# Kernel optimization log

Measured on AMD Instinct MI355X. Metric: run time of the kernel, lower is better.

Reference implementation:

```python
import jax, jax.numpy as jnp
import numpy as np

NUM_VIEW = 300
NSAMPLE = 1024
EPS = 1e-5


def generate_grasp_views(n):
    # golden-spiral views on the unit sphere (graspnetAPI.generate_grasp_views)
    phi = (np.sqrt(5.0) - 1.0) / 2.0
    i = np.arange(n)
    zi = (2 * i + 1) / n - 1
    ri = np.sqrt(np.maximum(1 - zi ** 2, 0))
    xi = ri * np.cos(2 * np.pi * i * phi)
    yi = ri * np.sin(2 * np.pi * i * phi)
    return jnp.asarray(np.stack([xi, yi, zi], axis=-1).astype(np.float32))


def viewpoint_to_matrix(towards):
    # batch_viewpoint_params_to_matrix with angle=0 -> R1 = I
    axis_x = towards  # [M,3]
    axis_y = jnp.stack([-axis_x[:, 1], axis_x[:, 0], jnp.zeros_like(axis_x[:, 0])], axis=-1)
    ny = jnp.linalg.norm(axis_y, axis=-1, keepdims=True)
    axis_y = jnp.where(ny == 0, jnp.array([0.0, 1.0, 0.0], dtype=towards.dtype), axis_y)
    axis_x = axis_x / jnp.linalg.norm(axis_x, axis=-1, keepdims=True)
    axis_y = axis_y / jnp.linalg.norm(axis_y, axis=-1, keepdims=True)
    axis_z = jnp.cross(axis_x, axis_y)
    return jnp.stack([axis_x, axis_y, axis_z], axis=-1)  # columns = axes


def conv1x1(x, w, b):
    # x [B,C,N], w [O,C], b [O] -> [B,O,N]
    return jnp.einsum('oc,bcn->bon', w, x) + b[None, :, None]


def bn(x, g, be, m, v):
    # inference-mode BatchNorm1d over channel dim
    return (x - m[None, :, None]) * (g / jnp.sqrt(v + EPS))[None, :, None] + be[None, :, None]


def masked_fps(xyz, mask):
    # furthest point sampling restricted to mask==True; equivalent to running
    # standard FPS on the compacted point set (same points, same distances,
    # same selection order, indices expressed in original coordinates).
    big = jnp.float32(1e10)
    dist0 = jnp.where(mask, big, jnp.float32(-1.0))
    start = jnp.argmax(mask)  # first valid index == compacted index 0

    def step(carry, _):
        dist, cur = carry
        d = jnp.sum((xyz - xyz[cur]) ** 2, axis=-1)
        dist = jnp.where(mask, jnp.minimum(dist, d), jnp.float32(-1.0))
        nxt = jnp.argmax(dist)
        return (dist, nxt), cur

    _, inds = jax.lax.scan(step, (dist0, start), None, length=NSAMPLE)
    return inds  # [NSAMPLE]


def setup_inputs() -> dict:
    key = jax.random.key(0)
    ks = jax.random.split(key, 32)
    B, N, C, V = 4, 20000, 256, 300
    s = 0.05
    rn = lambda k, sh, sc=1.0: jax.random.normal(k, sh, jnp.float32) * sc
    rv = lambda k, sh: jax.random.uniform(k, sh, jnp.float32) + 0.5
    return {
        'seed_xyz': jax.random.uniform(ks[0], (B, N, 3), jnp.float32),
        'seed_features': rn(ks[1], (B, C, N)),
        # graspable_head: conv-bn-relu-conv
        'gh_w1': rn(ks[2], (C, C), s), 'gh_b1': rn(ks[3], (C,), s),
        'gh_g1': 1.0 + rn(ks[4], (C,), 0.1), 'gh_be1': rn(ks[5], (C,), 0.1),
        'gh_m1': rn(ks[6], (C,), 0.1), 'gh_v1': rv(ks[7], (C,)),
        'gh_w2': rn(ks[8], (3, C), s), 'gh_b2': rn(ks[9], (3,), s),
        # conv1 + bn1
        'w1': rn(ks[10], (C, C), s), 'b1': rn(ks[11], (C,), s),
        'g1': 1.0 + rn(ks[12], (C,), 0.1), 'be1': rn(ks[13], (C,), 0.1),
        'm1': rn(ks[14], (C,), 0.1), 'v1': rv(ks[15], (C,)),
        # conv2 + bn2
        'w2': rn(ks[16], (V, C), s), 'b2': rn(ks[17], (V,), s),
        'g2': 1.0 + rn(ks[18], (V,), 0.1), 'be2': rn(ks[19], (V,), 0.1),
        'm2': rn(ks[20], (V,), 0.1), 'v2': rv(ks[21], (V,)),
        # conv3
        'w3': rn(ks[22], (V, V), s), 'b3': rn(ks[23], (V,), s),
    }


def reference(seed_xyz, seed_features, gh_w1, gh_b1, gh_g1, gh_be1, gh_m1, gh_v1,
              gh_w2, gh_b2, w1, b1, g1, be1, m1, v1, w2, b2, g2, be2, m2, v2, w3, b3):
    B, N, _ = seed_xyz.shape
    # graspable head
    h = jax.nn.relu(bn(conv1x1(seed_features, gh_w1, gh_b1), gh_g1, gh_be1, gh_m1, gh_v1))
    graspable = conv1x1(h, gh_w2, gh_b2)  # [B,3,N]
    objectness_score = graspable[:, :2]
    graspness_score = graspable[:, 2]  # [B,N]
    objectness_mask = jnp.argmax(objectness_score, axis=1) == 1
    graspness_mask = (graspness_score > 0.1) & objectness_mask
    # per-batch masked FPS to 1024 points
    inds = jax.vmap(masked_fps)(seed_xyz, graspness_mask)  # [B,1024]
    graspable_xyz = jnp.take_along_axis(seed_xyz, inds[:, :, None], axis=1)  # [B,1024,3]
    graspable_features = jnp.take_along_axis(seed_features, inds[:, None, :], axis=2)  # [B,C,1024]
    fp2_graspness = jnp.take_along_axis(graspness_score, inds, axis=1)  # [B,1024]
    # view head
    f = jax.nn.relu(bn(conv1x1(graspable_features, w1, b1), g1, be1, m1, v1))
    f = jax.nn.relu(bn(conv1x1(f, w2, b2), g2, be2, m2, v2))
    f = conv1x1(f, w3, b3)  # [B,V,1024]
    view_score = jnp.transpose(f, (0, 2, 1))  # [B,1024,V]
    top_view_scores = jnp.max(view_score, axis=2)
    top_view_inds = jnp.argmax(view_score, axis=2)
    templates = generate_grasp_views(NUM_VIEW)  # [V,3]
    vp_xyz = templates[top_view_inds]  # [B,1024,3]
    vp_rot = viewpoint_to_matrix((-vp_xyz).reshape(-1, 3)).reshape(B, NSAMPLE, 3, 3)
    return (graspness_score, objectness_mask, graspable_xyz, inds, graspable_features,
            fp2_graspness, view_score, top_view_inds, top_view_scores, vp_xyz, vp_rot)
```

## Files before the change

kernel.cpp:

```cpp
#include <hip/hip_runtime.h>
#include <math.h>

#define BB 4
#define NN 20000
#define CC 256
#define VV 300
#define SS 1024
#define CPKS 20480
#define W1MAX 3072

#define O_GRASP   0
#define O_OBJ     80000
#define O_GXYZ    160000
#define O_INDS    172288
#define O_GFEAT   176384
#define O_FPG     1224960
#define O_VIEW    1229056
#define O_TVI     2457856
#define O_TVS     2461952
#define O_VPX     2466048
#define O_VPR     2478336

#define W_GH1T    0
#define W_W1T     65536
#define W_W2T     131072
#define W_W3T     212992
#define W_TMPL    308992
#define W_SGH     309892
#define W_SC1     310148
#define W_SC2     310404
#define W_CNT     310704
#define W_CPK     310720
#define W_INDS    638400
#define W_MASK    642496
#define W_F1      722496
#define W_F2      1771072
#define W_F3      2999872

#define FMA4(A, W, X) do { \
    A.x = fmaf((W), (X).x, A.x); \
    A.y = fmaf((W), (X).y, A.y); \
    A.z = fmaf((W), (X).z, A.z); \
    A.w = fmaf((W), (X).w, A.w); } while (0)

__device__ __forceinline__ float4 bnrelu4(float4 a, float bb, float mm, float ssv, float ee) {
    float4 r;
    r.x = fmaxf(__fadd_rn(__fmul_rn(__fsub_rn(__fadd_rn(a.x, bb), mm), ssv), ee), 0.0f);
    r.y = fmaxf(__fadd_rn(__fmul_rn(__fsub_rn(__fadd_rn(a.y, bb), mm), ssv), ee), 0.0f);
    r.z = fmaxf(__fadd_rn(__fmul_rn(__fsub_rn(__fadd_rn(a.z, bb), mm), ssv), ee), 0.0f);
    r.w = fmaxf(__fadd_rn(__fmul_rn(__fsub_rn(__fadd_rn(a.w, bb), mm), ssv), ee), 0.0f);
    return r;
}

template <int CTRL>
__device__ __forceinline__ unsigned long long wmax_step(unsigned long long k) {
    int lo = (int)(unsigned int)k;
    int hi = (int)(unsigned int)(k >> 32);
    int plo = __builtin_amdgcn_update_dpp(lo, lo, CTRL, 0xf, 0xf, false);
    int phi = __builtin_amdgcn_update_dpp(hi, hi, CTRL, 0xf, 0xf, false);
    unsigned long long p = ((unsigned long long)(unsigned int)phi << 32) | (unsigned int)plo;
    return (p > k) ? p : k;
}
__device__ __forceinline__ unsigned long long wave_max_u64(unsigned long long k) {
    k = wmax_step<0x111>(k);
    k = wmax_step<0x112>(k);
    k = wmax_step<0x114>(k);
    k = wmax_step<0x118>(k);
    k = wmax_step<0x142>(k);
    k = wmax_step<0x143>(k);
    unsigned int lo = (unsigned int)__builtin_amdgcn_readlane((int)(unsigned int)k, 63);
    unsigned int hi = (unsigned int)__builtin_amdgcn_readlane((int)(unsigned int)(k >> 32), 63);
    return ((unsigned long long)hi << 32) | lo;
}

template <int N> struct Pts {
    Pts<N - 1> rest;
    float px, py, pz, dist;
    unsigned int klo;
};
template <> struct Pts<0> {};

template <int N, int SH, int J0>
__device__ __forceinline__ void pts_load(Pts<N>& P, const float4* __restrict__ base,
                                         int t, int M,
                                         unsigned long long& bkey, float& bx, float& by, float& bz) {
    if constexpr (N > 0) {
        pts_load<N - 1, SH, J0>(P.rest, base, t, M, bkey, bx, by, bz);
        constexpr int J = J0 + N - 1;
        if ((J << SH) < M) {
            float4 v = base[t + (J << SH)];
            P.px = v.x; P.py = v.y; P.pz = v.z;
            P.klo = __float_as_uint(v.w);
            P.dist = (P.klo != 0u) ? 1e10f : 0.0f;
            unsigned long long k = ((unsigned long long)__float_as_uint(P.dist) << 32) | P.klo;
            if (k > bkey) { bkey = k; bx = v.x; by = v.y; bz = v.z; }
        } else {
            P.px = P.py = P.pz = 0.0f; P.dist = 0.0f; P.klo = 0u;
        }
    }
}

template <int N, int SH, int J0>
__device__ __forceinline__ void pts_upd(Pts<N>& P, int t, int M,
                                        float cx, float cy, float cz,
                                        unsigned long long& bkey, float& bx, float& by, float& bz) {
    if constexpr (N > 0) {
        pts_upd<N - 1, SH, J0>(P.rest, t, M, cx, cy, cz, bkey, bx, by, bz);
        constexpr int J = J0 + N - 1;
        if ((J << SH) < M) {
            float dx = __fsub_rn(P.px, cx);
            float dy = __fsub_rn(P.py, cy);
            float dz = __fsub_rn(P.pz, cz);
            float d = __fadd_rn(__fadd_rn(__fmul_rn(dx, dx), __fmul_rn(dy, dy)), __fmul_rn(dz, dz));
            float nd = fminf(P.dist, d);
            P.dist = nd;
            unsigned long long k = ((unsigned long long)__float_as_uint(nd) << 32) | P.klo;
            if (k > bkey) { bkey = k; bx = P.px; by = P.py; bz = P.pz; }
        }
    }
}

__global__ void k0_prep(const float* __restrict__ w_gh1, const float* __restrict__ w1,
                        const float* __restrict__ w2, const float* __restrict__ w3,
                        const float* __restrict__ gh_g, const float* __restrict__ gh_v,
                        const float* __restrict__ g1, const float* __restrict__ v1,
                        const float* __restrict__ g2, const float* __restrict__ v2,
                        float* __restrict__ ws) {
    int id = blockIdx.x * 256 + threadIdx.x;
    if (id < 65536) {
        int k = id & 255, o = id >> 8;
        ws[W_GH1T + k * 256 + o] = w_gh1[id];
    } else if (id < 131072) {
        int l = id - 65536; int k = l & 255, o = l >> 8;
        ws[W_W1T + k * 256 + o] = w1[l];
    } else if (id < 207872) {
        int l = id - 131072; int k = l & 255, o = l >> 8;
        ws[W_W2T + k * 320 + o] = w2[l];
    } else if (id < 297872) {
        int l = id - 207872; int k = l % 300, o = l / 300;
        ws[W_W3T + k * 320 + o] = w3[l];
    } else if (id < 298172) {
        int i = id - 297872;
        double phi = (sqrt(5.0) - 1.0) / 2.0;
        double zi = (2.0 * (double)i + 1.0) / 300.0 - 1.0;
        double r2 = 1.0 - zi * zi; if (r2 < 0.0) r2 = 0.0;
        double ri = sqrt(r2);
        double th = (6.283185307179586 * (double)i) * phi;
        ws[W_TMPL + i * 3 + 0] = (float)(ri * cos(th));
        ws[W_TMPL + i * 3 + 1] = (float)(ri * sin(th));
        ws[W_TMPL + i * 3 + 2] = (float)zi;
    } else if (id < 298428) {
        int i = id - 298172; ws[W_SGH + i] = gh_g[i] / sqrtf(gh_v[i] + 1e-5f);
    } else if (id < 298684) {
        int i = id - 298428; ws[W_SC1 + i] = g1[i] / sqrtf(v1[i] + 1e-5f);
    } else if (id < 298984) {
        int i = id - 298684; ws[W_SC2 + i] = g2[i] / sqrtf(v2[i] + 1e-5f);
    } else if (id < 298988) {
        ((int*)(ws + W_CNT))[id - 298984] = 0;
    }
}

__global__ __launch_bounds__(256)
__attribute__((amdgpu_waves_per_eu(2, 2)))
void k1_stageA(
    const float* __restrict__ x,
    const float* __restrict__ wt,
    const float* __restrict__ b1g, const float* __restrict__ scg,
    const float* __restrict__ m1g, const float* __restrict__ be1g,
    const float* __restrict__ w2g, const float* __restrict__ b2g,
    float* __restrict__ out_grasp, float* __restrict__ out_obj, int* __restrict__ maskw) {
    __shared__ __align__(16) float Xs[256 * 64];
    int b = blockIdx.y;
    int n0 = blockIdx.x * 64;
    int t = threadIdx.x;
    const float* xb = x + (size_t)b * CC * NN;
    #pragma unroll
    for (int k = 0; k < 16; k++) {
        int id = t + k * 256; int c = id >> 4; int u = id & 15;
        int n = n0 + u * 4;
        float4 v = make_float4(0.f, 0.f, 0.f, 0.f);
        if (n < NN) v = *(const float4*)(xb + (size_t)c * NN + n);
        *(float4*)(Xs + c * 64 + u * 4) = v;
    }
    __syncthreads();
    int og = (t >> 3) * 8;
    int n8 = (t & 7) * 8;
    float4 a0l = {0,0,0,0}, a0h = {0,0,0,0}, a1l = {0,0,0,0}, a1h = {0,0,0,0};
    float4 a2l = {0,0,0,0}, a2h = {0,0,0,0}, a3l = {0,0,0,0}, a3h = {0,0,0,0};
    float4 a4l = {0,0,0,0}, a4h = {0,0,0,0}, a5l = {0,0,0,0}, a5h = {0,0,0,0};
    float4 a6l = {0,0,0,0}, a6h = {0,0,0,0}, a7l = {0,0,0,0}, a7h = {0,0,0,0};
    #pragma unroll 2
    for (int c = 0; c < 256; c++) {
        float4 wva = *(const float4*)(wt + c * 256 + og);
        float4 wvb = *(const float4*)(wt + c * 256 + og + 4);
        float4 xva = *(const float4*)(Xs + c * 64 + n8);
        float4 xvb = *(const float4*)(Xs + c * 64 + n8 + 4);
        FMA4(a0l, wva.x, xva); FMA4(a0h, wva.x, xvb);
        FMA4(a1l, wva.y, xva); FMA4(a1h, wva.y, xvb);
        FMA4(a2l, wva.z, xva); FMA4(a2h, wva.z, xvb);
        FMA4(a3l, wva.w, xva); FMA4(a3h, wva.w, xvb);
        FMA4(a4l, wvb.x, xva); FMA4(a4h, wvb.x, xvb);
        FMA4(a5l, wvb.y, xva); FMA4(a5h, wvb.y, xvb);
        FMA4(a6l, wvb.z, xva); FMA4(a6h, wvb.z, xvb);
        FMA4(a7l, wvb.w, xva); FMA4(a7h, wvb.w, xvb);
    }
    __syncthreads();
#define K1_EPI(I) { int o = og + I; \
    float bb = b1g[o], mm = m1g[o], ssv = scg[o], ee = be1g[o]; \
    *(float4*)(Xs + o * 64 + n8)     = bnrelu4(a##I##l, bb, mm, ssv, ee); \
    *(float4*)(Xs + o * 64 + n8 + 4) = bnrelu4(a##I##h, bb, mm, ssv, ee); }
    K1_EPI(0) K1_EPI(1) K1_EPI(2) K1_EPI(3)
    K1_EPI(4) K1_EPI(5) K1_EPI(6) K1_EPI(7)
#undef K1_EPI
    __syncthreads();
    if (t < 64) {
        float s0a = 0.0f, s1a = 0.0f, s2a = 0.0f;
        for (int c = 0; c < 256; c++) {
            float xv = Xs[c * 64 + t];
            s0a = fmaf(xv, w2g[c], s0a);
            s1a = fmaf(xv, w2g[256 + c], s1a);
            s2a = fmaf(xv, w2g[512 + c], s2a);
        }
        int n = n0 + t;
        if (n < NN) {
            float s0 = __fadd_rn(s0a, b2g[0]);
            float s1 = __fadd_rn(s1a, b2g[1]);
            float s2 = __fadd_rn(s2a, b2g[2]);
            bool obj = s1 > s0;
            bool gr = obj && (s2 > 0.1f);
            int gn = b * NN + n;
            out_grasp[gn] = s2;
            out_obj[gn] = obj ? 1.0f : 0.0f;
            maskw[gn] = gr ? 1 : 0;
        }
    }
}

__global__ void k2_compact(const float* __restrict__ sx, const int* __restrict__ maskr,
                           int* __restrict__ cnt, float4* __restrict__ cpk) {
    int n = blockIdx.x * 256 + threadIdx.x;
    int b = blockIdx.y;
    bool take = (n < NN) && (maskr[b * NN + n] != 0);
    unsigned long long m = __ballot(take);
    if (take) {
        int lane = threadIdx.x & 63;
        int lead = __ffsll((long long)m) - 1;
        int base = 0;
        if (lane == lead) base = atomicAdd(cnt + b, __popcll(m));
        base = __shfl(base, lead);
        int pos = base + __popcll(m & ((1ull << lane) - 1ull));
        const float* p = sx + ((size_t)b * NN + n) * 3;
        cpk[b * CPKS + pos] = make_float4(p[0], p[1], p[2], __uint_as_float(~(unsigned int)n));
    }
}

__global__ void k2_pad(const int* __restrict__ cnt, float4* __restrict__ cpk) {
    int b = blockIdx.x;
    int M = cnt[b];
    int Mpad = (M + 511) & ~511;
    for (int i = M + threadIdx.x; i < Mpad; i += 512)
        cpk[b * CPKS + i] = make_float4(0.f, 0.f, 0.f, __uint_as_float(0u));
}

template <int NCH>
__global__ __launch_bounds__(256)
__attribute__((amdgpu_waves_per_eu(1, 1)))
void k3_fps_w4(const float4* __restrict__ cpk,
               const int* __restrict__ cnt,
               float* __restrict__ out_inds,
               int* __restrict__ inds_i) {
    __shared__ unsigned long long skey[2][4];
    __shared__ __align__(16) float4 scd[2][4];
    __shared__ unsigned int res[SS];
    int b = blockIdx.x;
    int t = threadIdx.x;
    int wid = t >> 6, lane = t & 63;
    int M = __builtin_amdgcn_readfirstlane(cnt[b]);
    if constexpr (NCH == 2) {
        if (M == 0) {
            for (int s = t; s < SS; s += 256) { out_inds[b * SS + s] = 0.0f; inds_i[b * SS + s] = 0; }
            return;
        }
    }
    if (2 * ((M + 511) >> 9) != NCH) return;

    float px[NCH], py[NCH], pz[NCH], dist[NCH];
    unsigned int klo[NCH];
    unsigned long long bkey = 0ull;
    float bx = 0.0f, by = 0.0f, bz = 0.0f;
    const float4* gsrc = cpk + b * CPKS;
    #pragma unroll
    for (int j = 0; j < NCH; j++) {
        float4 v = gsrc[t + (j << 8)];
        px[j] = v.x; py[j] = v.y; pz[j] = v.z;
        klo[j] = __float_as_uint(v.w);
        dist[j] = (klo[j] != 0u) ? 1e10f : 0.0f;
        unsigned long long k = ((unsigned long long)__float_as_uint(dist[j]) << 32) | klo[j];
        bool g = k > bkey;
        bkey = g ? k : bkey;
        bx = g ? v.x : bx; by = g ? v.y : by; bz = g ? v.z : bz;
    }
    {
        unsigned long long wkey = wave_max_u64(bkey);
        unsigned long long mb = __ballot(bkey == wkey);
        if (lane == __ffsll((long long)mb) - 1) {
            skey[0][wid] = wkey;
            scd[0][wid] = make_float4(bx, by, bz, 0.0f);
        }
    }
    __syncthreads();
    int buf = 0;
    for (int step = 0; step < SS; step++) {
        unsigned long long wk = skey[buf][0];
        float4 c = scd[buf][0];
        #pragma unroll
        for (int i = 1; i < 4; i++) {
            unsigned long long k2 = skey[buf][i];
            float4 c2 = scd[buf][i];
            if (k2 > wk) { wk = k2; c = c2; }
        }
        if (t == 0) res[step] = (unsigned int)(wk & 0xFFFFFFFFull);
        if (step == SS - 1) break;
        float cx = c.x, cy = c.y, cz = c.z;
        bkey = 0ull; bx = by = bz = 0.0f;
        #pragma unroll
        for (int j = 0; j < NCH; j++) {
            float dx = __fsub_rn(px[j], cx);
            float dy = __fsub_rn(py[j], cy);
            float dz = __fsub_rn(pz[j], cz);
            float d = __fadd_rn(__fadd_rn(__fmul_rn(dx, dx), __fmul_rn(dy, dy)), __fmul_rn(dz, dz));
            float nd = fminf(dist[j], d);
            dist[j] = nd;
            unsigned long long k = ((unsigned long long)__float_as_uint(nd) << 32) | klo[j];
            bool g = k > bkey;
            bkey = g ? k : bkey;
            bx = g ? px[j] : bx; by = g ? py[j] : by; bz = g ? pz[j] : bz;
        }
        unsigned long long wkey = wave_max_u64(bkey);
        unsigned long long mb = __ballot(bkey == wkey);
        if (lane == __ffsll((long long)mb) - 1) {
            skey[buf ^ 1][wid] = wkey;
            scd[buf ^ 1][wid] = make_float4(bx, by, bz, 0.0f);
        }
        __syncthreads();
        buf ^= 1;
    }
    __syncthreads();
    for (int s = t; s < SS; s += 256) {
        unsigned int cid = ~res[s];
        out_inds[b * SS + s] = (float)cid;
        inds_i[b * SS + s] = (int)cid;
    }
}

template <int G>
__global__ __launch_bounds__(512)
__attribute__((amdgpu_waves_per_eu(2, 2)))
void k3_fps(const float4* __restrict__ cpk,
            const int* __restrict__ cnt,
            float* __restrict__ out_inds,
            int* __restrict__ inds_i, int minM) {
    int b = blockIdx.x;
    int t = threadIdx.x;
    int M = __builtin_amdgcn_readfirstlane(cnt[b]);
    if (M <= minM) return;
    __shared__ unsigned long long skey[2][8];
    __shared__ __align__(16) float4 scd[2][8];
    Pts<G> Pa, Pb;
    int wid = t >> 6, lane = t & 63;
    unsigned long long bkey = 0ull;
    float bx = 0, by = 0, bz = 0;
    const float4* base = cpk + b * CPKS;
    pts_load<G, 9, 0>(Pa, base, t, M, bkey, bx, by, bz);
    pts_load<G, 9, G>(Pb, base, t, M, bkey, bx, by, bz);
    {
        unsigned long long wkey = wave_max_u64(bkey);
        unsigned long long mb = __ballot(bkey == wkey);
        if (lane == __ffsll((long long)mb) - 1) {
            skey[0][wid] = wkey;
            scd[0][wid] = make_float4(bx, by, bz, 0.0f);
        }
    }
    __syncthreads();
    int buf = 0;
    for (int step = 0; step < SS; step++) {
        unsigned long long wk = skey[buf][0];
        float4 c = scd[buf][0];
        #pragma unroll
        for (int i = 1; i < 8; i++) {
            unsigned long long k2 = skey[buf][i];
            float4 c2 = scd[buf][i];
            if (k2 > wk) { wk = k2; c = c2; }
        }
        unsigned int cid = ~(unsigned int)(wk & 0xFFFFFFFFull);
        if (t == 0) { out_inds[b * SS + step] = (float)cid; inds_i[b * SS + step] = (int)cid; }
        bkey = 0ull; bx = by = bz = 0.0f;
        pts_upd<G, 9, 0>(Pa, t, M, c.x, c.y, c.z, bkey, bx, by, bz);
        pts_upd<G, 9, G>(Pb, t, M, c.x, c.y, c.z, bkey, bx, by, bz);
        unsigned long long wkey = wave_max_u64(bkey);
        unsigned long long mb = __ballot(bkey == wkey);
        if (lane == __ffsll((long long)mb) - 1) {
            skey[buf ^ 1][wid] = wkey;
            scd[buf ^ 1][wid] = make_float4(bx, by, bz, 0.0f);
        }
        __syncthreads();
        buf ^= 1;
    }
}

__global__ void k4_gatherF(const float* __restrict__ sf, const int* __restrict__ inds,
                           float* __restrict__ o_feat) {
    int id = blockIdx.x * 256 + threadIdx.x;
    int s = id & (SS - 1);
    int bc = id >> 10;
    int b = bc >> 8;
    int idx = inds[(b << 10) | s];
    o_feat[id] = sf[(size_t)bc * NN + idx];
}

__global__ void k4_gatherX(const float* __restrict__ sx, const int* __restrict__ inds,
                           const float* __restrict__ grasp_all,
                           float* __restrict__ o_xyz, float* __restrict__ o_fg) {
    int id = blockIdx.x * 256 + threadIdx.x;
    int b = id >> 10;
    int idx = inds[id];
    const float* p = sx + ((size_t)b * NN + idx) * 3;
    o_xyz[id * 3 + 0] = p[0];
    o_xyz[id * 3 + 1] = p[1];
    o_xyz[id * 3 + 2] = p[2];
    o_fg[id] = grasp_all[b * NN + idx];
}

__global__ __launch_bounds__(256)
__attribute__((amdgpu_waves_per_eu(2, 2)))
void k5_gemm(const float* __restrict__ X, const float* __restrict__ WT,
             const float* __restrict__ bias, const float* __restrict__ scale,
             const float* __restrict__ mean, const float* __restrict__ beta,
             float* __restrict__ Y, int O, int Opad, int K, int relu_bn) {
    __shared__ __align__(16) float Xs[64 * 64];
    int b = blockIdx.z;
    int n0 = blockIdx.y * 64;
    int o0 = blockIdx.x * 64;
    int t = threadIdx.x;
    int o4 = o0 + (t & 15) * 4;
    int n4 = (t >> 4) * 4;
    float4 ac0 = {0,0,0,0}, ac1 = {0,0,0,0}, ac2 = {0,0,0,0}, ac3 = {0,0,0,0};
    const float* Xb = X + (size_t)b * K * SS;
    for (int c0 = 0; c0 < K; c0 += 64) {
        #pragma unroll
        for (int k = 0; k < 4; k++) {
            int id = t + k * 256; int cc = id >> 4; int nn4 = (id & 15) * 4;
            int c = c0 + cc;
            float4 v = make_float4(0.f, 0.f, 0.f, 0.f);
            if (c < K) v = *(const float4*)(Xb + (size_t)c * SS + n0 + nn4);
            *(float4*)(Xs + cc * 64 + nn4) = v;
        }
        __syncthreads();
        int kmax = (K - c0 < 64) ? (K - c0) : 64;
        for (int cc = 0; cc < kmax; cc++) {
            float4 wv = *(const float4*)(WT + (size_t)(c0 + cc) * Opad + o4);
            float4 xv = *(const float4*)(Xs + cc * 64 + n4);
            FMA4(ac0, wv.x, xv);
            FMA4(ac1, wv.y, xv);
            FMA4(ac2, wv.z, xv);
            FMA4(ac3, wv.w, xv);
        }
        __syncthreads();
    }
#define K5_EPI(I) { int o = o4 + I; if (o < O) { \
    float bb = bias[o]; float4 v; \
    if (relu_bn) { v = bnrelu4(ac##I, bb, mean[o], scale[o], beta[o]); } \
    else { v.x = __fadd_rn(ac##I.x, bb); v.y = __fadd_rn(ac##I.y, bb); \
           v.z = __fadd_rn(ac##I.z, bb); v.w = __fadd_rn(ac##I.w, bb); } \
    *(float4*)(Y + ((size_t)b * O + o) * SS + n0 + n4) = v; } }
    K5_EPI(0) K5_EPI(1) K5_EPI(2) K5_EPI(3)
#undef K5_EPI
}

__global__ void k6_view(const float* __restrict__ Vs,
                        const float* __restrict__ tmpl,
                        float* __restrict__ o_ti, float* __restrict__ o_ts,
                        float* __restrict__ o_vx, float* __restrict__ o_vr) {
    int id = blockIdx.x * 256 + threadIdx.x;
    const float* f = Vs + (size_t)id * VV;
    float best = f[0];
    int bi = 0;
    for (int v = 1; v < VV; v++) {
        float x = f[v];
        if (x > best) { best = x; bi = v; }
    }
    o_ti[id] = (float)bi;
    o_ts[id] = best;
    float tx = tmpl[bi * 3 + 0], ty = tmpl[bi * 3 + 1], tz = tmpl[bi * 3 + 2];
    o_vx[id * 3 + 0] = tx; o_vx[id * 3 + 1] = ty; o_vx[id * 3 + 2] = tz;
    float ax0 = -tx, ax1 = -ty, ax2 = -tz;
    float ay0 = ty, ay1 = -tx, ay2 = 0.0f;
    float ny = sqrtf(__fadd_rn(__fadd_rn(__fmul_rn(ay0, ay0), __fmul_rn(ay1, ay1)), __fmul_rn(ay2, ay2)));
    if (ny == 0.0f) { ay0 = 0.0f; ay1 = 1.0f; ay2 = 0.0f; }
    float nx = sqrtf(__fadd_rn(__fadd_rn(__fmul_rn(ax0, ax0), __fmul_rn(ax1, ax1)), __fmul_rn(ax2, ax2)));
    ax0 = ax0 / nx; ax1 = ax1 / nx; ax2 = ax2 / nx;
    float ny2 = sqrtf(__fadd_rn(__fadd_rn(__fmul_rn(ay0, ay0), __fmul_rn(ay1, ay1)), __fmul_rn(ay2, ay2)));
    ay0 = ay0 / ny2; ay1 = ay1 / ny2; ay2 = ay2 / ny2;
    float az0 = __fsub_rn(__fmul_rn(ax1, ay2), __fmul_rn(ax2, ay1));
    float az1 = __fsub_rn(__fmul_rn(ax2, ay0), __fmul_rn(ax0, ay2));
    float az2 = __fsub_rn(__fmul_rn(ax0, ay1), __fmul_rn(ax1, ay0));
    float* R = o_vr + (size_t)id * 9;
    R[0] = ax0; R[1] = ay0; R[2] = az0;
    R[3] = ax1; R[4] = ay1; R[5] = az1;
    R[6] = ax2; R[7] = ay2; R[8] = az2;
}

__global__ void k7_transpose(const float* __restrict__ F3v, float* __restrict__ outp) {
    __shared__ float T[64][65];
    int b = blockIdx.z;
    int s0 = blockIdx.y * 64;
    int v0 = blockIdx.x * 64;
    int t = threadIdx.x;
    int sc = t & 63;
    int g = t >> 6;
    #pragma unroll
    for (int k = 0; k < 16; k++) {
        int vr = g * 16 + k;
        int v = v0 + vr;
        T[vr][sc] = (v < VV) ? F3v[((size_t)b * VV + v) * SS + s0 + sc] : 0.0f;
    }
    __syncthreads();
    #pragma unroll
    for (int k = 0; k < 16; k++) {
        int sr = g * 16 + k;
        int v = v0 + sc;
        if (v < VV)
            outp[((size_t)b * SS + (s0 + sr)) * VV + v] = T[sc][sr];
    }
}

extern "C" void kernel_launch(void* const* d_in, const int* in_sizes, int n_in,
                              void* d_out, int out_size, void* d_ws, size_t ws_size,
                              hipStream_t stream) {
    const float* seed_xyz  = (const float*)d_in[0];
    const float* seed_feat = (const float*)d_in[1];
    const float* gh_w1 = (const float*)d_in[2];
    const float* gh_b1 = (const float*)d_in[3];
    const float* gh_g1 = (const float*)d_in[4];
    const float* gh_be1 = (const float*)d_in[5];
    const float* gh_m1 = (const float*)d_in[6];
    const float* gh_v1 = (const float*)d_in[7];
    const float* gh_w2 = (const float*)d_in[8];
    const float* gh_b2 = (const float*)d_in[9];
    const float* w1 = (const float*)d_in[10];
    const float* b1 = (const float*)d_in[11];
    const float* g1 = (const float*)d_in[12];
    const float* be1 = (const float*)d_in[13];
    const float* m1 = (const float*)d_in[14];
    const float* v1 = (const float*)d_in[15];
    const float* w2 = (const float*)d_in[16];
    const float* b2 = (const float*)d_in[17];
    const float* g2 = (const float*)d_in[18];
    const float* be2 = (const float*)d_in[19];
    const float* m2 = (const float*)d_in[20];
    const float* v2 = (const float*)d_in[21];
    const float* w3 = (const float*)d_in[22];
    const float* b3 = (const float*)d_in[23];

    float* out = (float*)d_out;
    float* ws = (float*)d_ws;
    int* cnt = (int*)(ws + W_CNT);
    float4* cpk = (float4*)(ws + W_CPK);
    int* inds_i = (int*)(ws + W_INDS);
    int* maskw = (int*)(ws + W_MASK);

    k0_prep<<<dim3((298988 + 255) / 256), dim3(256), 0, stream>>>(
        gh_w1, w1, w2, w3, gh_g1, gh_v1, g1, v1, g2, v2, ws);

    k1_stageA<<<dim3((NN + 63) / 64, BB), dim3(256), 0, stream>>>(
        seed_feat, ws + W_GH1T, gh_b1, ws + W_SGH, gh_m1, gh_be1, gh_w2, gh_b2,
        out + O_GRASP, out + O_OBJ, maskw);

    k2_compact<<<dim3((NN + 255) / 256, BB), dim3(256), 0, stream>>>(seed_xyz, maskw, cnt, cpk);
    k2_pad<<<dim3(BB), dim3(512), 0, stream>>>(cnt, cpk);

    k3_fps_w4<2><<<dim3(BB), dim3(256), 0, stream>>>(cpk, cnt, out + O_INDS, inds_i);
    k3_fps_w4<4><<<dim3(BB), dim3(256), 0, stream>>>(cpk, cnt, out + O_INDS, inds_i);
    k3_fps_w4<6><<<dim3(BB), dim3(256), 0, stream>>>(cpk, cnt, out + O_INDS, inds_i);
    k3_fps_w4<8><<<dim3(BB), dim3(256), 0, stream>>>(cpk, cnt, out + O_INDS, inds_i);
    k3_fps_w4<10><<<dim3(BB), dim3(256), 0, stream>>>(cpk, cnt, out + O_INDS, inds_i);
    k3_fps_w4<12><<<dim3(BB), dim3(256), 0, stream>>>(cpk, cnt, out + O_INDS, inds_i);
    k3_fps<20><<<dim3(BB), dim3(512), 0, stream>>>(cpk, cnt, out + O_INDS, inds_i, W1MAX);

    k4_gatherF<<<dim3(BB * CC * SS / 256), dim3(256), 0, stream>>>(seed_feat, inds_i, out + O_GFEAT);
    k4_gatherX<<<dim3(BB * SS / 256), dim3(256), 0, stream>>>(
        seed_xyz, inds_i, out + O_GRASP, out + O_GXYZ, out + O_FPG);

    k5_gemm<<<dim3(4, 16, BB), dim3(256), 0, stream>>>(
        out + O_GFEAT, ws + W_W1T, b1, ws + W_SC1, m1, be1, ws + W_F1, 256, 256, 256, 1);
    k5_gemm<<<dim3(5, 16, BB), dim3(256), 0, stream>>>(
        ws + W_F1, ws + W_W2T, b2, ws + W_SC2, m2, be2, ws + W_F2, 300, 320, 256, 1);
    k5_gemm<<<dim3(5, 16, BB), dim3(256), 0, stream>>>(
        ws + W_F2, ws + W_W3T, b3, b3, b3, b3, ws + W_F3, 300, 320, 300, 0);

    k7_transpose<<<dim3(5, 16, BB), dim3(256), 0, stream>>>(ws + W_F3, out + O_VIEW);

    k6_view<<<dim3(BB * SS / 256), dim3(256), 0, stream>>>(
        out + O_VIEW, ws + W_TMPL, out + O_TVI, out + O_TVS, out + O_VPX, out + O_VPR);
}
```

Measured before the change: 1.186 ms.

## Widen FPS to 8 waves, fuse view transpose into GEMM, vectorize argmax

The masked-FPS kernel moves from 4 to 8 wavefronts per block, which halves the points each thread holds per step. The cost is an 8-way shared-memory reduction per step instead of 4, and the ballot-based single-writer election is replaced by a plain key-equality test. The last 1x1-conv GEMM now writes its output directly in [B,S,V] layout, which removes the separate transpose kernel and its intermediate buffer. The per-row view argmax reads float4 vectors and is unrolled.

After: 1.469 ms. 1.24x slower.

```diff
diff --git a/kernel.cpp b/kernel.cpp
--- a/kernel.cpp
+++ b/kernel.cpp
@@ -35,7 +35,6 @@
 #define W_MASK    642496
 #define W_F1      722496
 #define W_F2      1771072
-#define W_F3      2999872
 
 #define FMA4(A, W, X) do { \
     A.x = fmaf((W), (X).x, A.x); \
@@ -263,26 +262,26 @@
 }
 
 template <int NCH>
-__global__ __launch_bounds__(256)
-__attribute__((amdgpu_waves_per_eu(1, 1)))
-void k3_fps_w4(const float4* __restrict__ cpk,
+__global__ __launch_bounds__(512)
+__attribute__((amdgpu_waves_per_eu(2, 2)))
+void k3_fps_w8(const float4* __restrict__ cpk,
                const int* __restrict__ cnt,
                float* __restrict__ out_inds,
                int* __restrict__ inds_i) {
-    __shared__ unsigned long long skey[2][4];
-    __shared__ __align__(16) float4 scd[2][4];
+    __shared__ unsigned long long skey[2][8];
+    __shared__ __align__(16) float4 scd[2][8];
     __shared__ unsigned int res[SS];
     int b = blockIdx.x;
     int t = threadIdx.x;
-    int wid = t >> 6, lane = t & 63;
+    int wid = t >> 6;
     int M = __builtin_amdgcn_readfirstlane(cnt[b]);
-    if constexpr (NCH == 2) {
+    if constexpr (NCH == 1) {
         if (M == 0) {
-            for (int s = t; s < SS; s += 256) { out_inds[b * SS + s] = 0.0f; inds_i[b * SS + s] = 0; }
+            for (int s = t; s < SS; s += 512) { out_inds[b * SS + s] = 0.0f; inds_i[b * SS + s] = 0; }
             return;
         }
     }
-    if (2 * ((M + 511) >> 9) != NCH) return;
+    if (((M + 511) >> 9) != NCH) return;
 
     float px[NCH], py[NCH], pz[NCH], dist[NCH];
     unsigned int klo[NCH];
@@ -291,7 +290,7 @@
     const float4* gsrc = cpk + b * CPKS;
     #pragma unroll
     for (int j = 0; j < NCH; j++) {
-        float4 v = gsrc[t + (j << 8)];
+        float4 v = gsrc[t + (j << 9)];
         px[j] = v.x; py[j] = v.y; pz[j] = v.z;
         klo[j] = __float_as_uint(v.w);
         dist[j] = (klo[j] != 0u) ? 1e10f : 0.0f;
@@ -302,8 +301,7 @@
     }
     {
         unsigned long long wkey = wave_max_u64(bkey);
-        unsigned long long mb = __ballot(bkey == wkey);
-        if (lane == __ffsll((long long)mb) - 1) {
+        if (bkey == wkey) {
             skey[0][wid] = wkey;
             scd[0][wid] = make_float4(bx, by, bz, 0.0f);
         }
@@ -314,7 +312,7 @@
         unsigned long long wk = skey[buf][0];
         float4 c = scd[buf][0];
         #pragma unroll
-        for (int i = 1; i < 4; i++) {
+        for (int i = 1; i < 8; i++) {
             unsigned long long k2 = skey[buf][i];
             float4 c2 = scd[buf][i];
             if (k2 > wk) { wk = k2; c = c2; }
@@ -337,8 +335,7 @@
             bx = g ? px[j] : bx; by = g ? py[j] : by; bz = g ? pz[j] : bz;
         }
         unsigned long long wkey = wave_max_u64(bkey);
-        unsigned long long mb = __ballot(bkey == wkey);
-        if (lane == __ffsll((long long)mb) - 1) {
+        if (bkey == wkey) {
             skey[buf ^ 1][wid] = wkey;
             scd[buf ^ 1][wid] = make_float4(bx, by, bz, 0.0f);
         }
@@ -346,7 +343,7 @@
         buf ^= 1;
     }
     __syncthreads();
-    for (int s = t; s < SS; s += 256) {
+    for (int s = t; s < SS; s += 512) {
         unsigned int cid = ~res[s];
         out_inds[b * SS + s] = (float)cid;
         inds_i[b * SS + s] = (int)cid;
@@ -477,17 +474,70 @@
 #undef K5_EPI
 }
 
+__global__ __launch_bounds__(256)
+__attribute__((amdgpu_waves_per_eu(2, 2)))
+void k5_gemm_t(const float* __restrict__ X, const float* __restrict__ WT,
+               const float* __restrict__ bias,
+               float* __restrict__ Y, int Opad, int K) {
+    __shared__ __align__(16) float Xs[64 * 64];
+    int b = blockIdx.z;
+    int n0 = blockIdx.y * 64;
+    int o0 = blockIdx.x * 64;
+    int t = threadIdx.x;
+    int o4 = o0 + (t & 15) * 4;
+    int n4 = (t >> 4) * 4;
+    float4 ac0 = {0,0,0,0}, ac1 = {0,0,0,0}, ac2 = {0,0,0,0}, ac3 = {0,0,0,0};
+    const float* Xb = X + (size_t)b * K * SS;
+    for (int c0 = 0; c0 < K; c0 += 64) {
+        #pragma unroll
+        for (int k = 0; k < 4; k++) {
+            int id = t + k * 256; int cc = id >> 4; int nn4 = (id & 15) * 4;
+            int c = c0 + cc;
+            float4 v = make_float4(0.f, 0.f, 0.f, 0.f);
+            if (c < K) v = *(const float4*)(Xb + (size_t)c * SS + n0 + nn4);
+            *(float4*)(Xs + cc * 64 + nn4) = v;
+        }
+        __syncthreads();
+        int kmax = (K - c0 < 64) ? (K - c0) : 64;
+        for (int cc = 0; cc < kmax; cc++) {
+            float4 wv = *(const float4*)(WT + (size_t)(c0 + cc) * Opad + o4);
+            float4 xv = *(const float4*)(Xs + cc * 64 + n4);
+            FMA4(ac0, wv.x, xv);
+            FMA4(ac1, wv.y, xv);
+            FMA4(ac2, wv.z, xv);
+            FMA4(ac3, wv.w, xv);
+        }
+        __syncthreads();
+    }
+    if (o4 + 3 < VV) {
+        float4 bb4 = *(const float4*)(bias + o4);
+#define K5T_ROW(J, CMP) { \
+        float4 r; \
+        r.x = __fadd_rn(ac0.CMP, bb4.x); \
+        r.y = __fadd_rn(ac1.CMP, bb4.y); \
+        r.z = __fadd_rn(ac2.CMP, bb4.z); \
+        r.w = __fadd_rn(ac3.CMP, bb4.w); \
+        *(float4*)(Y + ((size_t)b * SS + (n0 + n4 + J)) * VV + o4) = r; }
+        K5T_ROW(0, x) K5T_ROW(1, y) K5T_ROW(2, z) K5T_ROW(3, w)
+#undef K5T_ROW
+    }
+}
+
 __global__ void k6_view(const float* __restrict__ Vs,
                         const float* __restrict__ tmpl,
                         float* __restrict__ o_ti, float* __restrict__ o_ts,
                         float* __restrict__ o_vx, float* __restrict__ o_vr) {
     int id = blockIdx.x * 256 + threadIdx.x;
-    const float* f = Vs + (size_t)id * VV;
-    float best = f[0];
+    const float4* f4 = (const float4*)(Vs + (size_t)id * VV);
+    float best = -INFINITY;
     int bi = 0;
-    for (int v = 1; v < VV; v++) {
-        float x = f[v];
-        if (x > best) { best = x; bi = v; }
+    #pragma unroll 5
+    for (int g = 0; g < VV / 4; g++) {
+        float4 x4 = f4[g];
+        if (x4.x > best) { best = x4.x; bi = g * 4; }
+        if (x4.y > best) { best = x4.y; bi = g * 4 + 1; }
+        if (x4.z > best) { best = x4.z; bi = g * 4 + 2; }
+        if (x4.w > best) { best = x4.w; bi = g * 4 + 3; }
     }
     o_ti[id] = (float)bi;
     o_ts[id] = best;
@@ -508,30 +558,6 @@
     R[0] = ax0; R[1] = ay0; R[2] = az0;
     R[3] = ax1; R[4] = ay1; R[5] = az1;
     R[6] = ax2; R[7] = ay2; R[8] = az2;
-}
-
-__global__ void k7_transpose(const float* __restrict__ F3v, float* __restrict__ outp) {
-    __shared__ float T[64][65];
-    int b = blockIdx.z;
-    int s0 = blockIdx.y * 64;
-    int v0 = blockIdx.x * 64;
-    int t = threadIdx.x;
-    int sc = t & 63;
-    int g = t >> 6;
-    #pragma unroll
-    for (int k = 0; k < 16; k++) {
-        int vr = g * 16 + k;
-        int v = v0 + vr;
-        T[vr][sc] = (v < VV) ? F3v[((size_t)b * VV + v) * SS + s0 + sc] : 0.0f;
-    }
-    __syncthreads();
-    #pragma unroll
-    for (int k = 0; k < 16; k++) {
-        int sr = g * 16 + k;
-        int v = v0 + sc;
-        if (v < VV)
-            outp[((size_t)b * SS + (s0 + sr)) * VV + v] = T[sc][sr];
-    }
 }
 
 extern "C" void kernel_launch(void* const* d_in, const int* in_sizes, int n_in,
@@ -579,12 +605,12 @@
     k2_compact<<<dim3((NN + 255) / 256, BB), dim3(256), 0, stream>>>(seed_xyz, maskw, cnt, cpk);
     k2_pad<<<dim3(BB), dim3(512), 0, stream>>>(cnt, cpk);
 
-    k3_fps_w4<2><<<dim3(BB), dim3(256), 0, stream>>>(cpk, cnt, out + O_INDS, inds_i);
-    k3_fps_w4<4><<<dim3(BB), dim3(256), 0, stream>>>(cpk, cnt, out + O_INDS, inds_i);
-    k3_fps_w4<6><<<dim3(BB), dim3(256), 0, stream>>>(cpk, cnt, out + O_INDS, inds_i);
-    k3_fps_w4<8><<<dim3(BB), dim3(256), 0, stream>>>(cpk, cnt, out + O_INDS, inds_i);
-    k3_fps_w4<10><<<dim3(BB), dim3(256), 0, stream>>>(cpk, cnt, out + O_INDS, inds_i);
-    k3_fps_w4<12><<<dim3(BB), dim3(256), 0, stream>>>(cpk, cnt, out + O_INDS, inds_i);
+    k3_fps_w8<1><<<dim3(BB), dim3(512), 0, stream>>>(cpk, cnt, out + O_INDS, inds_i);
+    k3_fps_w8<2><<<dim3(BB), dim3(512), 0, stream>>>(cpk, cnt, out + O_INDS, inds_i);
+    k3_fps_w8<3><<<dim3(BB), dim3(512), 0, stream>>>(cpk, cnt, out + O_INDS, inds_i);
+    k3_fps_w8<4><<<dim3(BB), dim3(512), 0, stream>>>(cpk, cnt, out + O_INDS, inds_i);
+    k3_fps_w8<5><<<dim3(BB), dim3(512), 0, stream>>>(cpk, cnt, out + O_INDS, inds_i);
+    k3_fps_w8<6><<<dim3(BB), dim3(512), 0, stream>>>(cpk, cnt, out + O_INDS, inds_i);
     k3_fps<20><<<dim3(BB), dim3(512), 0, stream>>>(cpk, cnt, out + O_INDS, inds_i, W1MAX);
 
     k4_gatherF<<<dim3(BB * CC * SS / 256), dim3(256), 0, stream>>>(seed_feat, inds_i, out + O_GFEAT);
@@ -595,10 +621,8 @@
         out + O_GFEAT, ws + W_W1T, b1, ws + W_SC1, m1, be1, ws + W_F1, 256, 256, 256, 1);
     k5_gemm<<<dim3(5, 16, BB), dim3(256), 0, stream>>>(
         ws + W_F1, ws + W_W2T, b2, ws + W_SC2, m2, be2, ws + W_F2, 300, 320, 256, 1);
-    k5_gemm<<<dim3(5, 16, BB), dim3(256), 0, stream>>>(
-        ws + W_F2, ws + W_W3T, b3, b3, b3, b3, ws + W_F3, 300, 320, 300, 0);
-
-    k7_transpose<<<dim3(5, 16, BB), dim3(256), 0, stream>>>(ws + W_F3, out + O_VIEW);
+    k5_gemm_t<<<dim3(5, 16, BB), dim3(256), 0, stream>>>(
+        ws + W_F2, ws + W_W3T, b3, out + O_VIEW, 320, 300);
 
     k6_view<<<dim3(BB * SS / 256), dim3(256), 0, stream>>>(
         out + O_VIEW, ws + W_TMPL, out + O_TVI, out + O_TVS, out + O_VPX, out + O_VPR);
```
